# Optimization experiments

Measured on AMD Instinct MI355X. Metric: run time of the kernel, lower is better.

The kernel has to match this reference:

```python
import jax, jax.numpy as jnp
import numpy as np

B, T, H, K = 64, 512, 768, 11
START_ID, END_ID = 9, 10  # tag_to_ix['<CLS>'], tag_to_ix['<SEP>']
NEG = -10000.0


def setup_inputs() -> dict:
    key = jax.random.key(0)
    k1, k2, k3, k4 = jax.random.split(key, 4)
    embeds = jax.random.normal(k1, (B, T, H), dtype=jnp.float32)
    W_fc = jax.random.normal(k2, (K, H), dtype=jnp.float32) * 0.02
    b_fc = jax.random.normal(k3, (K,), dtype=jnp.float32) * 0.02
    transitions = jax.random.normal(k4, (K, K), dtype=jnp.float32)
    # __init__ masking: no transition out of anything into START row, none into END col
    transitions = transitions.at[START_ID, :].set(NEG)
    transitions = transitions.at[:, END_ID].set(NEG)
    return {"embeds": embeds, "W_fc": W_fc, "b_fc": b_fc, "transitions": transitions}


def reference(embeds, W_fc, b_fc, transitions):
    # fc projection: feats[b,t,k] (PLM_crf path: encoder output -> Linear)
    feats = jnp.einsum('bth,kh->btk', embeds, W_fc) + b_fc  # [B,T,K]
    Bv, Tv, Kv = feats.shape

    # Viterbi: log_delta init -10000 except start tag; NOTE the original never
    # adds feats[:, 0] (loop starts at t=1), so we faithfully skip it too.
    log_delta0 = jnp.full((Bv, Kv), NEG, dtype=feats.dtype).at[:, START_ID].set(0.0)

    def step(log_delta, feat_t):
        # transitions[i, j]: score of moving from prev tag j to tag i
        scores = transitions[None, :, :] + log_delta[:, None, :]  # [B,K,K]
        psi_t = jnp.argmax(scores, axis=-1)                       # [B,K] best prev tag
        log_delta_new = jnp.max(scores, axis=-1) + feat_t         # [B,K]
        return log_delta_new, psi_t

    feats_seq = jnp.swapaxes(feats[:, 1:], 0, 1)                  # [T-1,B,K]
    log_delta, psi = jax.lax.scan(step, log_delta0, feats_seq)    # psi: [T-1,B,K]

    score = jnp.max(log_delta, axis=-1)                           # [B]
    last_tag = jnp.argmax(log_delta, axis=-1)                     # [B]

    # Backtrack: path[t] = psi[t+1][path[t+1]] for t = T-2 .. 0
    def back(next_tag, psi_t):
        tag = jnp.take_along_axis(psi_t, next_tag[:, None], axis=-1)[:, 0]
        return tag, tag

    _, path_rest = jax.lax.scan(back, last_tag, psi, reverse=True)  # [T-1,B]
    path = jnp.concatenate([jnp.swapaxes(path_rest, 0, 1), last_tag[:, None]], axis=1)  # [B,T]
    return score, path
```

## Files before the change

kernel.cpp:

```cpp
#include <hip/hip_runtime.h>

#define BB 64
#define TT 512
#define HH 768
#define KK 11
#define START_ID 9
#define NEGV -10000.0f

typedef float vf2 __attribute__((ext_vector_type(2)));

template <int CTRL>
__device__ __forceinline__ float dpp_add(float x) {
    int yi = __builtin_amdgcn_update_dpp(0, __float_as_int(x), CTRL, 0xF, 0xF, false);
    return x + __int_as_float(yi);
}

__device__ __forceinline__ float wave_sum_to_lane63(float x) {
    x = dpp_add<0x111>(x);
    x = dpp_add<0x112>(x);
    x = dpp_add<0x114>(x);
    x = dpp_add<0x118>(x);
    x = dpp_add<0x142>(x);
    x = dpp_add<0x143>(x);
    return x;
}

__device__ __forceinline__ float rlane(float v, int l) {
    return __int_as_float(__builtin_amdgcn_readlane(__float_as_int(v), l));
}

__global__ __launch_bounds__(256) void fc_kernel(const float* __restrict__ embeds,
                                                 const float* __restrict__ W,
                                                 const float* __restrict__ bias,
                                                 float* __restrict__ feats) {
    const int lane = threadIdx.x & 63;
    const int wave_id = (blockIdx.x * blockDim.x + threadIdx.x) >> 6;

    float4 wf[KK][3];
#pragma unroll
    for (int k = 0; k < KK; ++k)
#pragma unroll
        for (int r = 0; r < 3; ++r)
            wf[k][r] = *reinterpret_cast<const float4*>(W + k * HH + r * 256 + lane * 4);

    float bk[KK];
#pragma unroll
    for (int k = 0; k < KK; ++k) bk[k] = bias[k];

    const int base = wave_id * 8;
#pragma unroll 1
    for (int rr = 0; rr < 8; rr += 2) {
        const float* ea = embeds + (size_t)(base + rr) * HH;
        const float* eb = ea + HH;
        float4 a0 = *reinterpret_cast<const float4*>(ea + 0   + lane * 4);
        float4 a1 = *reinterpret_cast<const float4*>(ea + 256 + lane * 4);
        float4 a2 = *reinterpret_cast<const float4*>(ea + 512 + lane * 4);
        float4 b0 = *reinterpret_cast<const float4*>(eb + 0   + lane * 4);
        float4 b1 = *reinterpret_cast<const float4*>(eb + 256 + lane * 4);
        float4 b2 = *reinterpret_cast<const float4*>(eb + 512 + lane * 4);

        vf2 va[6] = {{a0.x, a0.y}, {a0.z, a0.w}, {a1.x, a1.y},
                     {a1.z, a1.w}, {a2.x, a2.y}, {a2.z, a2.w}};
        vf2 vb[6] = {{b0.x, b0.y}, {b0.z, b0.w}, {b1.x, b1.y},
                     {b1.z, b1.w}, {b2.x, b2.y}, {b2.z, b2.w}};

        float rA[KK], rB[KK];
#pragma unroll
        for (int k = 0; k < KK; ++k) {
            vf2 wv[6] = {{wf[k][0].x, wf[k][0].y}, {wf[k][0].z, wf[k][0].w},
                         {wf[k][1].x, wf[k][1].y}, {wf[k][1].z, wf[k][1].w},
                         {wf[k][2].x, wf[k][2].y}, {wf[k][2].z, wf[k][2].w}};
            vf2 sA = va[0] * wv[0];
            vf2 sB = vb[0] * wv[0];
#pragma unroll
            for (int r = 1; r < 6; ++r) { sA += va[r] * wv[r]; sB += vb[r] * wv[r]; }
            rA[k] = wave_sum_to_lane63(sA.x + sA.y);
            rB[k] = wave_sum_to_lane63(sB.x + sB.y);
        }
        if (lane == 63) {
            float* oA = feats + (size_t)(base + rr) * KK;
#pragma unroll
            for (int k = 0; k < KK; ++k) oA[k] = rA[k] + bk[k];
#pragma unroll
            for (int k = 0; k < KK; ++k) oA[KK + k] = rB[k] + bk[k];
        }
    }
}

__global__ __launch_bounds__(256) void viterbi_kernel(const float* __restrict__ feats,
                                                      const float* __restrict__ trans,
                                                      float* __restrict__ out) {
    __shared__ __align__(16) float feats_lds[(TT + 4) * KK];
    __shared__ __align__(16) float dh[(TT - 1) * 12];
    __shared__ int psi_lds[(TT - 1) * KK];
    __shared__ float tr_lds[KK * KK];
    __shared__ int comp[15 * KK];
    __shared__ int bt[16];
    __shared__ int sh_last;

    const int tid = threadIdx.x;
    const int b = blockIdx.x;

    {
        const float4* src = reinterpret_cast<const float4*>(feats + (size_t)b * TT * KK);
        float4* dst = reinterpret_cast<float4*>(feats_lds);
        for (int i = tid; i < TT * KK / 4; i += 256) dst[i] = src[i];
        if (tid < KK * KK) tr_lds[tid] = trans[tid];
    }
    __syncthreads();

    if (tid < 64) {
        const int i = tid;
        const int ci = (i < KK) ? i : 0;
        float tr[KK];
#pragma unroll
        for (int j = 0; j < KK; ++j) tr[j] = (i < KK) ? tr_lds[i * KK + j] : NEGV;

        float delta = (i == START_ID) ? 0.0f : NEGV;

        auto vstep = [&](int t, float fcur) {
            if (i < KK) dh[(t - 1) * 12 + i] = delta;
            float dj[KK];
#pragma unroll
            for (int j = 0; j < KK; ++j) dj[j] = rlane(delta, j);
            float s[KK];
#pragma unroll
            for (int j = 0; j < KK; ++j) s[j] = tr[j] + dj[j];
            float t0 = fmaxf(fmaxf(s[0], s[1]), s[2]);
            float t1 = fmaxf(fmaxf(s[3], s[4]), s[5]);
            float t2 = fmaxf(fmaxf(s[6], s[7]), s[8]);
            float t3 = fmaxf(s[9], s[10]);
            float best = fmaxf(fmaxf(fmaxf(t0, t1), t2), t3);
            delta = best + fcur;
        };

        float fr0 = feats_lds[1 * KK + ci];
        float fr1 = feats_lds[2 * KK + ci];
        float fr2 = feats_lds[3 * KK + ci];
        float fr3 = feats_lds[4 * KK + ci];

        int t = 1;
#pragma unroll 1
        for (; t <= TT - 4; t += 4) {
            vstep(t,     fr0); fr0 = feats_lds[(t + 4) * KK + ci];
            vstep(t + 1, fr1); fr1 = feats_lds[(t + 5) * KK + ci];
            vstep(t + 2, fr2); fr2 = feats_lds[(t + 6) * KK + ci];
            vstep(t + 3, fr3); fr3 = feats_lds[(t + 7) * KK + ci];
        }
        vstep(TT - 3, fr0);
        vstep(TT - 2, fr1);
        vstep(TT - 1, fr2);

        float dfin[KK];
#pragma unroll
        for (int j = 0; j < KK; ++j) dfin[j] = rlane(delta, j);
        float best = dfin[0];
        int last = 0;
#pragma unroll
        for (int j = 1; j < KK; ++j) {
            bool c = dfin[j] > best;
            best = c ? dfin[j] : best;
            last = c ? j : last;
        }
        if (tid == 0) {
            out[b] = best;
            out[BB + (size_t)b * TT + (TT - 1)] = (float)last;
            sh_last = last;
        }
    }
    __syncthreads();

    {
        const int i = tid & 15;
        const int sg = tid >> 4;
        if (i < KK) {
            float tri[KK];
#pragma unroll
            for (int j = 0; j < KK; ++j) tri[j] = tr_lds[i * KK + j];
            for (int s = sg; s < TT - 1; s += 16) {
                const float4* dr = reinterpret_cast<const float4*>(dh + s * 12);
                float4 a = dr[0], c4 = dr[1], d4 = dr[2];
                float sc[KK] = {tri[0] + a.x,  tri[1] + a.y,  tri[2] + a.z,  tri[3] + a.w,
                                tri[4] + c4.x, tri[5] + c4.y, tri[6] + c4.z, tri[7] + c4.w,
                                tri[8] + d4.x, tri[9] + d4.y, tri[10] + d4.z};
                float bv = sc[0];
                int bj = 0;
#pragma unroll
                for (int j = 1; j < KK; ++j) {
                    bool c = sc[j] > bv;
                    bv = c ? sc[j] : bv;
                    bj = c ? j : bj;
                }
                psi_lds[s * KK + i] = bj;
            }
        }
    }
    __syncthreads();

    {
        const int c = tid >> 4;
        const int i = tid & 15;
        if (c < 15 && i < KK) {
            int cur = i;
            for (int s = c * 32 + 31; s >= c * 32; --s) cur = psi_lds[s * KK + cur];
            comp[c * KK + i] = cur;
        } else if (c == 15 && i == 0) {
            int cur = sh_last;
            float* po = out + BB + (size_t)b * TT;
            for (int s = TT - 2; s >= 480; --s) {
                cur = psi_lds[s * KK + cur];
                po[s] = (float)cur;
            }
            bt[15] = cur;
        }
    }
    __syncthreads();

    if (tid == 0) {
        for (int c = 14; c >= 1; --c) bt[c] = comp[c * KK + bt[c + 1]];
    }
    __syncthreads();

    if (tid < 15) {
        const int c = tid;
        int cur = bt[c + 1];
        float* po = out + BB + (size_t)b * TT;
        for (int s = c * 32 + 31; s >= c * 32; --s) {
            cur = psi_lds[s * KK + cur];
            po[s] = (float)cur;
        }
    }
}

extern "C" void kernel_launch(void* const* d_in, const int* in_sizes, int n_in,
                              void* d_out, int out_size, void* d_ws, size_t ws_size,
                              hipStream_t stream) {
    const float* embeds = (const float*)d_in[0];
    const float* W_fc   = (const float*)d_in[1];
    const float* b_fc   = (const float*)d_in[2];
    const float* trans  = (const float*)d_in[3];
    float* out = (float*)d_out;
    float* feats = (float*)d_ws;

    fc_kernel<<<1024, 256, 0, stream>>>(embeds, W_fc, b_fc, feats);
    viterbi_kernel<<<BB, 256, 0, stream>>>(feats, trans, out);
}
```

Baseline: 202.9 us.

## Fuse FC projection into Viterbi kernel with 512-thread blocks per sequence

```diff
diff --git a/kernel.cpp b/kernel.cpp
--- a/kernel.cpp
+++ b/kernel.cpp
@@ -9,12 +9,15 @@
 
 typedef float vf2 __attribute__((ext_vector_type(2)));
 
+__device__ __forceinline__ float rlane(float v, int l) {
+    return __int_as_float(__builtin_amdgcn_readlane(__float_as_int(v), l));
+}
+
 template <int CTRL>
 __device__ __forceinline__ float dpp_add(float x) {
     int yi = __builtin_amdgcn_update_dpp(0, __float_as_int(x), CTRL, 0xF, 0xF, false);
     return x + __int_as_float(yi);
 }
-
 __device__ __forceinline__ float wave_sum_to_lane63(float x) {
     x = dpp_add<0x111>(x);
     x = dpp_add<0x112>(x);
@@ -25,71 +28,11 @@
     return x;
 }
 
-__device__ __forceinline__ float rlane(float v, int l) {
-    return __int_as_float(__builtin_amdgcn_readlane(__float_as_int(v), l));
-}
-
-__global__ __launch_bounds__(256) void fc_kernel(const float* __restrict__ embeds,
-                                                 const float* __restrict__ W,
-                                                 const float* __restrict__ bias,
-                                                 float* __restrict__ feats) {
-    const int lane = threadIdx.x & 63;
-    const int wave_id = (blockIdx.x * blockDim.x + threadIdx.x) >> 6;
-
-    float4 wf[KK][3];
-#pragma unroll
-    for (int k = 0; k < KK; ++k)
-#pragma unroll
-        for (int r = 0; r < 3; ++r)
-            wf[k][r] = *reinterpret_cast<const float4*>(W + k * HH + r * 256 + lane * 4);
-
-    float bk[KK];
-#pragma unroll
-    for (int k = 0; k < KK; ++k) bk[k] = bias[k];
-
-    const int base = wave_id * 8;
-#pragma unroll 1
-    for (int rr = 0; rr < 8; rr += 2) {
-        const float* ea = embeds + (size_t)(base + rr) * HH;
-        const float* eb = ea + HH;
-        float4 a0 = *reinterpret_cast<const float4*>(ea + 0   + lane * 4);
-        float4 a1 = *reinterpret_cast<const float4*>(ea + 256 + lane * 4);
-        float4 a2 = *reinterpret_cast<const float4*>(ea + 512 + lane * 4);
-        float4 b0 = *reinterpret_cast<const float4*>(eb + 0   + lane * 4);
-        float4 b1 = *reinterpret_cast<const float4*>(eb + 256 + lane * 4);
-        float4 b2 = *reinterpret_cast<const float4*>(eb + 512 + lane * 4);
-
-        vf2 va[6] = {{a0.x, a0.y}, {a0.z, a0.w}, {a1.x, a1.y},
-                     {a1.z, a1.w}, {a2.x, a2.y}, {a2.z, a2.w}};
-        vf2 vb[6] = {{b0.x, b0.y}, {b0.z, b0.w}, {b1.x, b1.y},
-                     {b1.z, b1.w}, {b2.x, b2.y}, {b2.z, b2.w}};
-
-        float rA[KK], rB[KK];
-#pragma unroll
-        for (int k = 0; k < KK; ++k) {
-            vf2 wv[6] = {{wf[k][0].x, wf[k][0].y}, {wf[k][0].z, wf[k][0].w},
-                         {wf[k][1].x, wf[k][1].y}, {wf[k][1].z, wf[k][1].w},
-                         {wf[k][2].x, wf[k][2].y}, {wf[k][2].z, wf[k][2].w}};
-            vf2 sA = va[0] * wv[0];
-            vf2 sB = vb[0] * wv[0];
-#pragma unroll
-            for (int r = 1; r < 6; ++r) { sA += va[r] * wv[r]; sB += vb[r] * wv[r]; }
-            rA[k] = wave_sum_to_lane63(sA.x + sA.y);
-            rB[k] = wave_sum_to_lane63(sB.x + sB.y);
-        }
-        if (lane == 63) {
-            float* oA = feats + (size_t)(base + rr) * KK;
-#pragma unroll
-            for (int k = 0; k < KK; ++k) oA[k] = rA[k] + bk[k];
-#pragma unroll
-            for (int k = 0; k < KK; ++k) oA[KK + k] = rB[k] + bk[k];
-        }
-    }
-}
-
-__global__ __launch_bounds__(256) void viterbi_kernel(const float* __restrict__ feats,
-                                                      const float* __restrict__ trans,
-                                                      float* __restrict__ out) {
+__global__ __launch_bounds__(512, 2) void crf_fused(const float* __restrict__ embeds,
+                                                    const float* __restrict__ W,
+                                                    const float* __restrict__ bias,
+                                                    const float* __restrict__ trans,
+                                                    float* __restrict__ out) {
     __shared__ __align__(16) float feats_lds[(TT + 4) * KK];
     __shared__ __align__(16) float dh[(TT - 1) * 12];
     __shared__ int psi_lds[(TT - 1) * KK];
@@ -99,13 +42,65 @@
     __shared__ int sh_last;
 
     const int tid = threadIdx.x;
+    const int lane = tid & 63;
+    const int wv = tid >> 6;
     const int b = blockIdx.x;
 
+    if (tid < KK * KK) tr_lds[tid] = trans[tid];
+
     {
-        const float4* src = reinterpret_cast<const float4*>(feats + (size_t)b * TT * KK);
-        float4* dst = reinterpret_cast<float4*>(feats_lds);
-        for (int i = tid; i < TT * KK / 4; i += 256) dst[i] = src[i];
-        if (tid < KK * KK) tr_lds[tid] = trans[tid];
+        float4 wf[KK][3];
+#pragma unroll
+        for (int k = 0; k < KK; ++k)
+#pragma unroll
+            for (int r = 0; r < 3; ++r)
+                wf[k][r] = *reinterpret_cast<const float4*>(W + k * HH + r * 256 + lane * 4);
+
+        float bk[KK];
+#pragma unroll
+        for (int k = 0; k < KK; ++k) bk[k] = bias[k];
+
+        const float* ebase = embeds + (size_t)b * TT * HH;
+#pragma unroll 1
+        for (int it = 0; it < 32; ++it) {
+            const int r0 = wv * 64 + it * 2;
+            const float* ea = ebase + (size_t)r0 * HH;
+            const float* eb = ea + HH;
+            float4 a0 = *reinterpret_cast<const float4*>(ea + 0   + lane * 4);
+            float4 a1 = *reinterpret_cast<const float4*>(ea + 256 + lane * 4);
+            float4 a2 = *reinterpret_cast<const float4*>(ea + 512 + lane * 4);
+            float4 b0 = *reinterpret_cast<const float4*>(eb + 0   + lane * 4);
+            float4 b1 = *reinterpret_cast<const float4*>(eb + 256 + lane * 4);
+            float4 b2 = *reinterpret_cast<const float4*>(eb + 512 + lane * 4);
+
+            vf2 va[6] = {{a0.x, a0.y}, {a0.z, a0.w}, {a1.x, a1.y},
+                         {a1.z, a1.w}, {a2.x, a2.y}, {a2.z, a2.w}};
+            vf2 vb[6] = {{b0.x, b0.y}, {b0.z, b0.w}, {b1.x, b1.y},
+                         {b1.z, b1.w}, {b2.x, b2.y}, {b2.z, b2.w}};
+
+            float rA[KK], rB[KK];
+#pragma unroll
+            for (int k = 0; k < KK; ++k) {
+                vf2 wv0 = {wf[k][0].x, wf[k][0].y}, wv1 = {wf[k][0].z, wf[k][0].w};
+                vf2 wv2 = {wf[k][1].x, wf[k][1].y}, wv3 = {wf[k][1].z, wf[k][1].w};
+                vf2 wv4 = {wf[k][2].x, wf[k][2].y}, wv5 = {wf[k][2].z, wf[k][2].w};
+                vf2 sA = va[0] * wv0;
+                vf2 sB = vb[0] * wv0;
+                sA += va[1] * wv1;  sB += vb[1] * wv1;
+                sA += va[2] * wv2;  sB += vb[2] * wv2;
+                sA += va[3] * wv3;  sB += vb[3] * wv3;
+                sA += va[4] * wv4;  sB += vb[4] * wv4;
+                sA += va[5] * wv5;  sB += vb[5] * wv5;
+                rA[k] = wave_sum_to_lane63(sA.x + sA.y);
+                rB[k] = wave_sum_to_lane63(sB.x + sB.y);
+            }
+            if (lane == 63) {
+#pragma unroll
+                for (int k = 0; k < KK; ++k) feats_lds[r0 * KK + k] = rA[k] + bk[k];
+#pragma unroll
+                for (int k = 0; k < KK; ++k) feats_lds[(r0 + 1) * KK + k] = rB[k] + bk[k];
+            }
+        }
     }
     __syncthreads();
 
@@ -177,7 +172,7 @@
             float tri[KK];
 #pragma unroll
             for (int j = 0; j < KK; ++j) tri[j] = tr_lds[i * KK + j];
-            for (int s = sg; s < TT - 1; s += 16) {
+            for (int s = sg; s < TT - 1; s += 32) {
                 const float4* dr = reinterpret_cast<const float4*>(dh + s * 12);
                 float4 a = dr[0], c4 = dr[1], d4 = dr[2];
                 float sc[KK] = {tri[0] + a.x,  tri[1] + a.y,  tri[2] + a.z,  tri[3] + a.w,
@@ -240,8 +235,6 @@
     const float* b_fc   = (const float*)d_in[2];
     const float* trans  = (const float*)d_in[3];
     float* out = (float*)d_out;
-    float* feats = (float*)d_ws;
-
-    fc_kernel<<<1024, 256, 0, stream>>>(embeds, W_fc, b_fc, feats);
-    viterbi_kernel<<<BB, 256, 0, stream>>>(feats, trans, out);
-}
+
+    crf_fused<<<BB, 512, 0, stream>>>(embeds, W_fc, b_fc, trans, out);
+}
```

Measured after the change: 247.8 us. 22.1% more time.
